# Kernel optimization log

Hardware: AMD Instinct MI355X
Metric: run time of the kernel (lower is better)

Reference implementation:

```python
import jax, jax.numpy as jnp
import numpy as np

N_NODES = 20000
N_EDGES = 320000
N_GRAPHS = 256
HIDDEN = 128
L = 4
NUM_ATOM = 28
NUM_BOND = 4
AVG_LOG = float(np.log(17.0))  # avg degree 16 -> avg_d['log']
EPS = 1e-5


def setup_inputs() -> dict:
    key = jax.random.key(0)
    ks = jax.random.split(key, 16)
    D = HIDDEN
    return {
        "x": jax.random.randint(ks[0], (N_NODES,), 0, NUM_ATOM, dtype=jnp.int32),
        "batch": jnp.sort(jax.random.randint(ks[1], (N_NODES,), 0, N_GRAPHS, dtype=jnp.int32)),
        "edge_index": jax.random.randint(ks[2], (2, N_EDGES), 0, N_NODES, dtype=jnp.int32),
        "snorm_n": jax.random.uniform(ks[3], (N_NODES, 1), dtype=jnp.float32),
        "edge_attr": jax.random.randint(ks[4], (N_EDGES,), 0, NUM_BOND, dtype=jnp.int32),
        "atom_emb": jax.random.normal(ks[5], (NUM_ATOM, D), jnp.float32) * 0.1,
        "bond_emb": jax.random.normal(ks[6], (NUM_BOND, D), jnp.float32) * 0.1,
        "pre_W": jax.random.normal(ks[7], (L, 3 * D, D), jnp.float32) / np.sqrt(3 * D),
        "pre_b": jnp.zeros((L, D), jnp.float32),
        "post_W": jax.random.normal(ks[8], (L, 13 * D, D), jnp.float32) / np.sqrt(13 * D),
        "post_b": jnp.zeros((L, D), jnp.float32),
        "mix_W": jax.random.normal(ks[9], (L, D, D), jnp.float32) / np.sqrt(D),
        "mix_b": jnp.zeros((L, D), jnp.float32),
        "bn_gamma": jnp.ones((L, D), jnp.float32),
        "bn_beta": jnp.zeros((L, D), jnp.float32),
        "r_W1": jax.random.normal(ks[10], (D, D // 2), jnp.float32) / np.sqrt(D),
        "r_b1": jnp.zeros((D // 2,), jnp.float32),
        "r_W2": jax.random.normal(ks[11], (D // 2, D // 4), jnp.float32) / np.sqrt(D // 2),
        "r_b2": jnp.zeros((D // 4,), jnp.float32),
        "r_W3": jax.random.normal(ks[12], (D // 4, 1), jnp.float32) / np.sqrt(D // 4),
        "r_b3": jnp.zeros((1,), jnp.float32),
    }


def _pna_forward(x, batch, edge_index, snorm_n, edge_attr,
                 atom_emb, bond_emb, pre_W, pre_b, post_W, post_b,
                 mix_W, mix_b, bn_gamma, bn_beta,
                 r_W1, r_b1, r_W2, r_b2, r_W3, r_b3):
    src, dst = edge_index[0], edge_index[1]
    h = atom_emb[x]                          # [N, D]
    e = bond_emb[edge_attr]                  # [E, D]
    # in-degree and PNA degree scalers (computed once)
    d = jax.ops.segment_sum(jnp.ones((src.shape[0],), h.dtype), dst, N_NODES)
    has_nb = (d > 0)[:, None]
    d_safe = jnp.maximum(d, 1.0)[:, None]
    logd = jnp.log1p(d)[:, None]
    amp = logd / AVG_LOG                     # amplification scaler
    att = AVG_LOG / jnp.maximum(logd, EPS)   # attenuation scaler
    for l in range(L):
        h_in = h
        # pretrans on edges: FC(cat(h_dst, h_src, e)) with LeakyReLU
        m = jnp.concatenate([h[dst], h[src], e], axis=-1)            # [E, 3D]
        m = jax.nn.leaky_relu(m @ pre_W[l] + pre_b[l])               # [E, D]
        # aggregators: mean, max, min, std
        mean = jax.ops.segment_sum(m, dst, N_NODES) / d_safe
        mean_sq = jax.ops.segment_sum(m * m, dst, N_NODES) / d_safe
        std = jnp.where(has_nb, jnp.sqrt(jax.nn.relu(mean_sq - mean * mean) + EPS), 0.0)
        mx = jnp.where(has_nb, jax.ops.segment_max(m, dst, N_NODES), 0.0)
        mn = jnp.where(has_nb, jax.ops.segment_min(m, dst, N_NODES), 0.0)
        agg = jnp.concatenate([mean, mx, mn, std], axis=-1)          # [N, 4D]
        agg = jnp.concatenate([agg, agg * amp, agg * att], axis=-1)  # [N, 12D]
        # posttrans FC on cat(h, agg) + mixing FC
        ph = jax.nn.leaky_relu(jnp.concatenate([h, agg], axis=-1) @ post_W[l] + post_b[l])
        ph = jax.nn.leaky_relu(ph @ mix_W[l] + mix_b[l])
        ph = ph * snorm_n                    # graph_norm
        mu = ph.mean(axis=0)                 # BatchNorm (training-mode stats)
        var = ph.var(axis=0)
        ph = bn_gamma[l] * (ph - mu) * jax.lax.rsqrt(var + EPS) + bn_beta[l]
        h = h_in + ph                        # residual
    # global mean pool per graph
    cnt = jax.ops.segment_sum(jnp.ones((x.shape[0],), h.dtype), batch, N_GRAPHS)
    g = jax.ops.segment_sum(h, batch, N_GRAPHS) / jnp.maximum(cnt, 1.0)[:, None]
    # MLPReadout: D -> D/2 -> D/4 -> 1 with ReLU
    g = jax.nn.relu(g @ r_W1 + r_b1)
    g = jax.nn.relu(g @ r_W2 + r_b2)
    return g @ r_W3 + r_b3                   # [B, 1]


def reference(x, batch, edge_index, snorm_n, edge_attr,
              atom_emb, bond_emb, pre_W, pre_b, post_W, post_b,
              mix_W, mix_b, bn_gamma, bn_beta,
              r_W1, r_b1, r_W2, r_b2, r_W3, r_b3):
    return _pna_forward(x, batch, edge_index, snorm_n, edge_attr,
                        atom_emb, bond_emb, pre_W, pre_b, post_W, post_b,
                        mix_W, mix_b, bn_gamma, bn_beta,
                        r_W1, r_b1, r_W2, r_b2, r_W3, r_b3)
```

## Files before the change

kernel.cpp:

```cpp
#include <hip/hip_runtime.h>
#include <math.h>

#define N_NODES 20000
#define N_EDGES 320000
#define N_GRAPHS 256
#define HID 128
#define NLAYERS 4
#define AVG_LOG 2.833213344056216f
#define EPS 1e-5f
#define MB64 313
#define NPAD 20032
#define SCANB 20
#define PITCH 40

typedef __attribute__((ext_vector_type(8))) short short8;
typedef __attribute__((ext_vector_type(4))) float f32x4;

static __device__ __forceinline__ float leaky(float v){ return v > 0.f ? v : 0.01f*v; }

static __device__ __forceinline__ void bsplit(float f, unsigned short& hi, unsigned short& lo){
  unsigned int u = __float_as_uint(f);
  unsigned int r = u + 0x7FFFu + ((u>>16)&1u);
  hi = (unsigned short)(r>>16);
  float hf = __uint_as_float(((unsigned int)hi)<<16);
  float l = f - hf;
  unsigned int v = __float_as_uint(l);
  unsigned int s = v + 0x7FFFu + ((v>>16)&1u);
  lo = (unsigned short)(s>>16);
}

static __device__ __forceinline__ void bsplit4(float4 f, ushort4& h, ushort4& l){
  bsplit(f.x, h.x, l.x); bsplit(f.y, h.y, l.y);
  bsplit(f.z, h.z, l.z); bsplit(f.w, h.w, l.w);
}

static __device__ __forceinline__ void gload16(const void* g, void* l){
  __builtin_amdgcn_global_load_lds((const __attribute__((address_space(1))) void*)g,
                                   (__attribute__((address_space(3))) void*)l, 16, 0, 0);
}

__global__ void k_count(const int* __restrict__ dst, int* __restrict__ deg){
  int e = blockIdx.x*blockDim.x + threadIdx.x;
  if (e < N_EDGES) atomicAdd(&deg[dst[e]], 1);
}

__global__ __launch_bounds__(1024) void k_scan1(const int* __restrict__ deg,
                                                int* __restrict__ excl, int* __restrict__ btot){
  __shared__ int buf[1024];
  int b = blockIdx.x, tid = threadIdx.x;
  int i = b*1024 + tid;
  int v = (i < N_NODES) ? deg[i] : 0;
  buf[tid] = v;
  __syncthreads();
  for (int ofs = 1; ofs < 1024; ofs <<= 1){
    int t = (tid >= ofs) ? buf[tid-ofs] : 0;
    __syncthreads();
    buf[tid] += t;
    __syncthreads();
  }
  excl[i] = buf[tid] - v;
  if (tid == 1023) btot[b] = buf[1023];
}

__global__ __launch_bounds__(1024) void k_scan2(
    const int* __restrict__ deg, const int* __restrict__ excl, const int* __restrict__ btot,
    int* __restrict__ off, float* __restrict__ invd,
    float* __restrict__ amp, float* __restrict__ att){
  __shared__ int carry_s;
  int b = blockIdx.x, tid = threadIdx.x;
  if (tid == 0){
    int c = 0;
    for (int j = 0; j < b; ++j) c += btot[j];
    carry_s = c;
  }
  __syncthreads();
  int i = b*1024 + tid;
  if (i <= N_NODES){
    off[i] = carry_s + excl[i];
    if (i < N_NODES){
      float d = (float)deg[i];
      invd[i] = 1.f / fmaxf(d, 1.f);
      float ld = log1pf(d);
      amp[i] = ld / AVG_LOG;
      att[i] = AVG_LOG / fmaxf(ld, EPS);
    }
  }
}

__global__ void k_fill(const int* __restrict__ src, const int* __restrict__ dst,
                       const int* __restrict__ eattr, const int* __restrict__ off,
                       int* __restrict__ cursor,
                       int* __restrict__ srcS, int* __restrict__ eaS){
  int e = blockIdx.x*blockDim.x + threadIdx.x;
  if (e < N_EDGES){
    int d = dst[e];
    int pos = off[d] + atomicAdd(&cursor[d], 1);
    srcS[pos] = src[e]; eaS[pos] = eattr[e];
  }
}

__global__ void k_goff(const int* __restrict__ batch, int* __restrict__ goff){
  int g = threadIdx.x;
  if (g <= N_GRAPHS){
    int lo = 0, hi = N_NODES;
    while (lo < hi){ int mid = (lo+hi)>>1; if (batch[mid] < g) lo = mid+1; else hi = mid; }
    goff[g] = lo;
  }
}

__global__ void k_hinit(const int* __restrict__ x, const float* __restrict__ atom_emb,
                        float* __restrict__ h,
                        unsigned short* __restrict__ h16h, unsigned short* __restrict__ h16l){
  int idx = blockIdx.x*blockDim.x + threadIdx.x;
  if (idx < N_NODES*32){
    int n = idx >> 5, q = idx & 31;
    float4 v = ((const float4*)atom_emb)[(size_t)x[n]*32 + q];
    ((float4*)h)[(size_t)n*32 + q] = v;
    ushort4 hh, ll; bsplit4(v, hh, ll);
    *(ushort4*)(h16h + (size_t)n*128 + q*4) = hh;
    *(ushort4*)(h16l + (size_t)n*128 + q*4) = ll;
  }
}

__global__ void k_bondall(const float* __restrict__ bond_emb, const float* __restrict__ pre_W,
                          const float* __restrict__ pre_b, float* __restrict__ BW3all){
  int l = blockIdx.x, tid = threadIdx.x;
  int r = tid >> 7, c = tid & 127;
  const float* W3 = pre_W + (size_t)l*384*128 + 256*128;
  float s = pre_b[l*128 + c];
  for (int k = 0; k < 128; ++k) s = fmaf(bond_emb[r*128 + k], W3[k*128 + c], s);
  BW3all[l*512 + tid] = s;
}

__global__ void k_wt(const float* __restrict__ pre_W, const float* __restrict__ post_W,
                     const float* __restrict__ mix_W,
                     unsigned short* __restrict__ whi, unsigned short* __restrict__ wlo){
  int y = blockIdx.y; int l = y/7, j = y%7;
  int K = (j>=3 && j<6) ? 512 : 128;
  const float* src; size_t off;
  if (j < 2)      { src = pre_W  + (size_t)l*384*128  + (size_t)j*128*128;            off = (size_t)j*16384; }
  else if (j == 2){ src = post_W + (size_t)l*1664*128;                                off = 2*16384; }
  else if (j < 6) { src = post_W + (size_t)l*1664*128 + (size_t)(128+(j-3)*512)*128;  off = 49152 + (size_t)(j-3)*65536; }
  else            { src = mix_W  + (size_t)l*128*128;                                 off = 245760; }
  unsigned short* dh = whi + (size_t)l*262144 + off;
  unsigned short* dl = wlo + (size_t)l*262144 + off;
  int kq8 = K/8;
  int ntask = 128*kq8;
  int t = blockIdx.x*256 + threadIdx.x;
  if (t >= ntask) return;
  int c  = t / kq8;
  int k0 = (t % kq8)*8;
  unsigned short h8[8] __attribute__((aligned(16)));
  unsigned short l8[8] __attribute__((aligned(16)));
  #pragma unroll
  for (int i=0;i<8;++i) bsplit(src[(size_t)(k0+i)*128 + c], h8[i], l8[i]);
  *(uint4*)(dh + (size_t)c*K + k0) = *(const uint4*)h8;
  *(uint4*)(dl + (size_t)c*K + k0) = *(const uint4*)l8;
}

template<int MODE>
__global__ __launch_bounds__(256) void k_mf16(
    const unsigned short* __restrict__ whi, const unsigned short* __restrict__ wlo,
    const unsigned short* __restrict__ Ahg, const unsigned short* __restrict__ Alg,
    float* __restrict__ out)
{
  const int K    = (MODE==1) ? 512 : 128;
  const int ASTR = (MODE==1) ? 512 : 128;
  const int OSTR = (MODE==1) ? 384 : 128;
  __shared__ unsigned short Ah[64*32], Al[64*32], Bh[128*32], Bl[128*32];
  int tid = threadIdx.x;
  int lane = tid & 63;
  int wv = tid >> 6;
  int wm = (wv>>1)*32, wn = (wv&1)*64;
  int y = blockIdx.x % 3;
  int mbase = (blockIdx.x / 3) * 64;
  const unsigned short* wh = whi + (size_t)y*K*128;
  const unsigned short* wl = wlo + (size_t)y*K*128;
  float* outp = out; int ocol = 0;
  if (MODE == 0) outp = out + (size_t)y*(size_t)N_NODES*128;
  if (MODE == 1) ocol = y*128;

  int lq = lane >> 2, ls = lane & 3;
  int kg = ls ^ (lq & 3) ^ ((lq >> 2) & 3);
  int a_row = wv*16 + lq;
  const unsigned short* agh = Ahg + (size_t)(mbase + a_row)*ASTR + kg*8;
  const unsigned short* agl = Alg + (size_t)(mbase + a_row)*ASTR + kg*8;
  unsigned short* a_ldsh = Ah + wv*512;
  unsigned short* a_ldsl = Al + wv*512;
  int b_col0 = (wv*2+0)*16 + lq;
  int b_col1 = (wv*2+1)*16 + lq;
  const unsigned short* bgh0 = wh + (size_t)b_col0*K + kg*8;
  const unsigned short* bgh1 = wh + (size_t)b_col1*K + kg*8;
  const unsigned short* bgl0 = wl + (size_t)b_col0*K + kg*8;
  const unsigned short* bgl1 = wl + (size_t)b_col1*K + kg*8;
  unsigned short* b_ldsh0 = Bh + (wv*2+0)*512;
  unsigned short* b_ldsh1 = Bh + (wv*2+1)*512;
  unsigned short* b_ldsl0 = Bl + (wv*2+0)*512;
  unsigned short* b_ldsl1 = Bl + (wv*2+1)*512;

  f32x4 acc[2][4];
  #pragma unroll
  for (int mi=0;mi<2;++mi)
    #pragma unroll
    for (int ni=0;ni<4;++ni)
      acc[mi][ni] = (f32x4){0.f,0.f,0.f,0.f};

  int lr = lane & 15, lk = lane >> 4;
  int sl = lk ^ (lr & 3) ^ ((lr >> 2) & 3);

  for (int kt = 0; kt < K; kt += 32){
    gload16(agh + kt, a_ldsh);
    gload16(agl + kt, a_ldsl);
    gload16(bgh0 + kt, b_ldsh0);
    gload16(bgh1 + kt, b_ldsh1);
    gload16(bgl0 + kt, b_ldsl0);
    gload16(bgl1 + kt, b_ldsl1);
    __syncthreads();
    short8 ah[2], al2[2], bh4[4], bl4[4];
    #pragma unroll
    for (int mi=0;mi<2;++mi){
      int idx = (wm + mi*16 + lr)*32 + sl*8;
      ah[mi]  = *(const short8*)(Ah + idx);
      al2[mi] = *(const short8*)(Al + idx);
    }
    #pragma unroll
    for (int ni=0;ni<4;++ni){
      int idx = (wn + ni*16 + lr)*32 + sl*8;
      bh4[ni] = *(const short8*)(Bh + idx);
      bl4[ni] = *(const short8*)(Bl + idx);
    }
    #pragma unroll
    for (int mi=0;mi<2;++mi){
      #pragma unroll
      for (int ni=0;ni<4;++ni){
        acc[mi][ni] = __builtin_amdgcn_mfma_f32_16x16x32_bf16(ah[mi],  bh4[ni], acc[mi][ni], 0,0,0);
        acc[mi][ni] = __builtin_amdgcn_mfma_f32_16x16x32_bf16(ah[mi],  bl4[ni], acc[mi][ni], 0,0,0);
        acc[mi][ni] = __builtin_amdgcn_mfma_f32_16x16x32_bf16(al2[mi], bh4[ni], acc[mi][ni], 0,0,0);
      }
    }
    __syncthreads();
  }

  #pragma unroll
  for (int mi=0;mi<2;++mi){
    #pragma unroll
    for (int ni=0;ni<4;++ni){
      int gcol = wn + ni*16 + lr;
      #pragma unroll
      for (int r=0;r<4;++r){
        int grow = mbase + wm + mi*16 + lk*4 + r;
        if (grow < N_NODES)
          outp[(size_t)grow*OSTR + ocol + gcol] = acc[mi][ni][r];
      }
    }
  }
}

__global__ __launch_bounds__(256) void k_mix(
    const unsigned short* __restrict__ wh, const unsigned short* __restrict__ wl,
    const float* __restrict__ Yh, const float* __restrict__ Yamt,
    const float* __restrict__ amp, const float* __restrict__ att,
    const float* __restrict__ post_b, const float* __restrict__ mix_b,
    const float* __restrict__ snorm,
    float* __restrict__ tb, float* __restrict__ bnpart)
{
  __shared__ unsigned short Ah[64*PITCH], Al[64*PITCH], Bh[128*PITCH], Bl[128*PITCH];
  __shared__ float bns[2][128], bnq[2][128];
  int tid = threadIdx.x;
  int lane = tid & 63;
  int wv = tid >> 6;
  int wm = (wv>>1)*32, wn = (wv&1)*64;
  int mbase = blockIdx.x*64;

  int a_row = tid >> 2, a_kg = tid & 3;
  int a_nrow = min(mbase + a_row, N_NODES-1);
  float av = amp[a_nrow], tv2 = att[a_nrow];
  const float* yhp = Yh   + (size_t)a_nrow*128;
  const float* yap = Yamt + (size_t)a_nrow*384;
  unsigned short* a_dh = Ah + a_row*PITCH + a_kg*8;
  unsigned short* a_dl = Al + a_row*PITCH + a_kg*8;

  f32x4 acc[2][4];
  #pragma unroll
  for (int mi=0;mi<2;++mi)
    #pragma unroll
    for (int ni=0;ni<4;++ni)
      acc[mi][ni] = (f32x4){0.f,0.f,0.f,0.f};

  int lr = lane & 15, lk = lane >> 4;

  for (int kt = 0; kt < 128; kt += 32){
    #pragma unroll
    for (int i=0;i<2;++i){
      int s = tid + 256*i;
      int col = s >> 2, kgg = s & 3;
      *(uint4*)(Bh + col*PITCH + kgg*8) = *(const uint4*)(wh + (size_t)col*128 + kt + kgg*8);
      *(uint4*)(Bl + col*PITCH + kgg*8) = *(const uint4*)(wl + (size_t)col*128 + kt + kgg*8);
    }
    {
      int c0 = kt + a_kg*8;
      float4 h0 = *(const float4*)(yhp + c0),       h1 = *(const float4*)(yhp + c0 + 4);
      float4 a0 = *(const float4*)(yap + c0),       a1 = *(const float4*)(yap + c0 + 4);
      float4 m0 = *(const float4*)(yap + 128 + c0), m1 = *(const float4*)(yap + 132 + c0);
      float4 t0 = *(const float4*)(yap + 256 + c0), t1 = *(const float4*)(yap + 260 + c0);
      float4 p0 = *(const float4*)(post_b + c0),    p1 = *(const float4*)(post_b + c0 + 4);
      float fv[8];
      fv[0] = leaky(h0.x + a0.x + av*m0.x + tv2*t0.x + p0.x);
      fv[1] = leaky(h0.y + a0.y + av*m0.y + tv2*t0.y + p0.y);
      fv[2] = leaky(h0.z + a0.z + av*m0.z + tv2*t0.z + p0.z);
      fv[3] = leaky(h0.w + a0.w + av*m0.w + tv2*t0.w + p0.w);
      fv[4] = leaky(h1.x + a1.x + av*m1.x + tv2*t1.x + p1.x);
      fv[5] = leaky(h1.y + a1.y + av*m1.y + tv2*t1.y + p1.y);
      fv[6] = leaky(h1.z + a1.z + av*m1.z + tv2*t1.z + p1.z);
      fv[7] = leaky(h1.w + a1.w + av*m1.w + tv2*t1.w + p1.w);
      unsigned short h8[8] __attribute__((aligned(16)));
      unsigned short l8[8] __attribute__((aligned(16)));
      #pragma unroll
      for (int i=0;i<8;++i) bsplit(fv[i], h8[i], l8[i]);
      *(uint4*)a_dh = *(const uint4*)h8;
      *(uint4*)a_dl = *(const uint4*)l8;
    }
    __syncthreads();
    short8 ah[2], al2[2], bh4[4], bl4[4];
    #pragma unroll
    for (int mi=0;mi<2;++mi){
      int idx = (wm + mi*16 + lr)*PITCH + lk*8;
      ah[mi]  = *(const short8*)(Ah + idx);
      al2[mi] = *(const short8*)(Al + idx);
    }
    #pragma unroll
    for (int ni=0;ni<4;++ni){
      int idx = (wn + ni*16 + lr)*PITCH + lk*8;
      bh4[ni] = *(const short8*)(Bh + idx);
      bl4[ni] = *(const short8*)(Bl + idx);
    }
    #pragma unroll
    for (int mi=0;mi<2;++mi){
      #pragma unroll
      for (int ni=0;ni<4;++ni){
        acc[mi][ni] = __builtin_amdgcn_mfma_f32_16x16x32_bf16(ah[mi],  bh4[ni], acc[mi][ni], 0,0,0);
        acc[mi][ni] = __builtin_amdgcn_mfma_f32_16x16x32_bf16(ah[mi],  bl4[ni], acc[mi][ni], 0,0,0);
        acc[mi][ni] = __builtin_amdgcn_mfma_f32_16x16x32_bf16(al2[mi], bh4[ni], acc[mi][ni], 0,0,0);
      }
    }
    __syncthreads();
  }

  float sn[2][4]; bool vld[2][4];
  #pragma unroll
  for (int mi=0;mi<2;++mi)
    #pragma unroll
    for (int r=0;r<4;++r){
      int grow = mbase + wm + mi*16 + lk*4 + r;
      vld[mi][r] = (grow < N_NODES);
      sn[mi][r] = vld[mi][r] ? snorm[grow] : 0.f;
    }
  int half = wv >> 1;
  #pragma unroll
  for (int ni=0;ni<4;++ni){
    int gcol = wn + ni*16 + lr;
    float bv = mix_b[gcol];
    float s = 0.f, q = 0.f;
    #pragma unroll
    for (int mi=0;mi<2;++mi){
      #pragma unroll
      for (int r=0;r<4;++r){
        if (vld[mi][r]){
          int grow = mbase + wm + mi*16 + lk*4 + r;
          float v = leaky(acc[mi][ni][r] + bv) * sn[mi][r];
          tb[(size_t)grow*128 + gcol] = v;
          s += v; q += v*v;
        }
      }
    }
    s += __shfl_xor(s, 16); s += __shfl_xor(s, 32);
    q += __shfl_xor(q, 16); q += __shfl_xor(q, 32);
    if (lk == 0){ bns[half][gcol] = s; bnq[half][gcol] = q; }
  }
  __syncthreads();
  if (tid < 128){
    bnpart[(size_t)blockIdx.x*256 + tid]       = bns[0][tid] + bns[1][tid];
    bnpart[(size_t)blockIdx.x*256 + 128 + tid] = bnq[0][tid] + bnq[1][tid];
  }
}

__global__ __launch_bounds__(256) void k_fusedagg(
    const float* __restrict__ H1, const float* __restrict__ H2,
    const float* __restrict__ BW3,
    const int* __restrict__ srcS, const int* __restrict__ eaS,
    const int* __restrict__ off, const float* __restrict__ invd,
    unsigned short* __restrict__ aggh, unsigned short* __restrict__ aggl)
{
  __shared__ float bw[4][128];
  int tid = threadIdx.x;
  bw[tid>>7][tid&127]     = BW3[tid];
  bw[2+(tid>>7)][tid&127] = BW3[256+tid];
  __syncthreads();

  int node = blockIdx.x*8 + (tid>>5);
  int q = tid & 31;
  float4 c4 = ((const float4*)(H1 + (size_t)node*HID))[q];
  int s = off[node], e = off[node+1];
  float4 sum = make_float4(0,0,0,0), sq = make_float4(0,0,0,0);
  float4 mx = make_float4(-3.4e38f,-3.4e38f,-3.4e38f,-3.4e38f);
  float4 mn = make_float4( 3.4e38f, 3.4e38f, 3.4e38f, 3.4e38f);

  #define FA_BODY(T,B) { \
    float vx = leaky(c4.x + T.x + B.x); \
    float vy = leaky(c4.y + T.y + B.y); \
    float vz = leaky(c4.z + T.z + B.z); \
    float vw = leaky(c4.w + T.w + B.w); \
    sum.x += vx; sum.y += vy; sum.z += vz; sum.w += vw; \
    sq.x += vx*vx; sq.y += vy*vy; sq.z += vz*vz; sq.w += vw*vw; \
    mx.x = fmaxf(mx.x, vx); mx.y = fmaxf(mx.y, vy); mx.z = fmaxf(mx.z, vz); mx.w = fmaxf(mx.w, vw); \
    mn.x = fminf(mn.x, vx); mn.y = fminf(mn.y, vy); mn.z = fminf(mn.z, vz); mn.w = fminf(mn.w, vw); }

  int i = s;
  for (; i + 1 < e; i += 2){
    int sv0 = srcS[i],   ev0 = eaS[i];
    int sv1 = srcS[i+1], ev1 = eaS[i+1];
    float4 t0 = ((const float4*)(H2 + (size_t)sv0*HID))[q];
    float4 t1 = ((const float4*)(H2 + (size_t)sv1*HID))[q];
    float4 b0 = ((const float4*)(&bw[ev0][0]))[q];
    float4 b1 = ((const float4*)(&bw[ev1][0]))[q];
    FA_BODY(t0,b0)
    FA_BODY(t1,b1)
  }
  if (i < e){
    int sv = srcS[i], ev = eaS[i];
    float4 t  = ((const float4*)(H2 + (size_t)sv*HID))[q];
    float4 b4 = ((const float4*)(&bw[ev][0]))[q];
    FA_BODY(t,b4)
  }
  #undef FA_BODY

  bool has = (e > s);
  float iv = invd[node];
  float4 mean = make_float4(sum.x*iv, sum.y*iv, sum.z*iv, sum.w*iv);
  float4 msq  = make_float4(sq.x*iv,  sq.y*iv,  sq.z*iv,  sq.w*iv);
  float4 sd;
  sd.x = has ? sqrtf(fmaxf(msq.x - mean.x*mean.x, 0.f) + EPS) : 0.f;
  sd.y = has ? sqrtf(fmaxf(msq.y - mean.y*mean.y, 0.f) + EPS) : 0.f;
  sd.z = has ? sqrtf(fmaxf(msq.z - mean.z*mean.z, 0.f) + EPS) : 0.f;
  sd.w = has ? sqrtf(fmaxf(msq.w - mean.w*mean.w, 0.f) + EPS) : 0.f;
  if (!has){ mx = make_float4(0,0,0,0); mn = make_float4(0,0,0,0); }
  size_t base = (size_t)node*512 + q*4;
  ushort4 hh, ll;
  bsplit4(mean, hh, ll);
  *(ushort4*)(aggh + base      ) = hh; *(ushort4*)(aggl + base      ) = ll;
  bsplit4(mx, hh, ll);
  *(ushort4*)(aggh + base + 128) = hh; *(ushort4*)(aggl + base + 128) = ll;
  bsplit4(mn, hh, ll);
  *(ushort4*)(aggh + base + 256) = hh; *(ushort4*)(aggl + base + 256) = ll;
  bsplit4(sd, hh, ll);
  *(ushort4*)(aggh + base + 384) = hh; *(ushort4*)(aggl + base + 384) = ll;
}

__global__ __launch_bounds__(512) void k_bnfinal(const float* __restrict__ bnpart,
                                                 float* __restrict__ mu, float* __restrict__ rstd){
  __shared__ double ss[4][128], qq[4][128];
  int tid = threadIdx.x;
  int c = tid & 127, p = tid >> 7;
  double s = 0.0, q = 0.0;
  for (int b = p; b < MB64; b += 4){
    s += (double)bnpart[(size_t)b*256 + c];
    q += (double)bnpart[(size_t)b*256 + 128 + c];
  }
  ss[p][c] = s; qq[p][c] = q;
  __syncthreads();
  if (p == 0){
    double S = ss[0][c] + ss[1][c] + ss[2][c] + ss[3][c];
    double Q = qq[0][c] + qq[1][c] + qq[2][c] + qq[3][c];
    double mean = S / (double)N_NODES;
    double var  = Q / (double)N_NODES - mean*mean;
    mu[c] = (float)mean;
    rstd[c] = rsqrtf((float)var + EPS);
  }
}

__global__ void k_apply(const float* __restrict__ t, const float* __restrict__ mu,
                        const float* __restrict__ rstd, const float* __restrict__ gamma,
                        const float* __restrict__ beta, float* __restrict__ h,
                        unsigned short* __restrict__ h16h, unsigned short* __restrict__ h16l){
  int idx = blockIdx.x*blockDim.x + threadIdx.x;
  if (idx < N_NODES*32){
    int n = idx >> 5, q = idx & 31;
    float4 tv = ((const float4*)t)[(size_t)n*32 + q];
    float4 hv = ((float4*)h)[(size_t)n*32 + q];
    float4 g4 = ((const float4*)gamma)[q], b4 = ((const float4*)beta)[q];
    float4 m4 = ((const float4*)mu)[q],    r4 = ((const float4*)rstd)[q];
    hv.x += g4.x*(tv.x-m4.x)*r4.x + b4.x;
    hv.y += g4.y*(tv.y-m4.y)*r4.y + b4.y;
    hv.z += g4.z*(tv.z-m4.z)*r4.z + b4.z;
    hv.w += g4.w*(tv.w-m4.w)*r4.w + b4.w;
    ((float4*)h)[(size_t)n*32 + q] = hv;
    ushort4 hh, ll; bsplit4(hv, hh, ll);
    *(ushort4*)(h16h + (size_t)n*128 + q*4) = hh;
    *(ushort4*)(h16l + (size_t)n*128 + q*4) = ll;
  }
}

__global__ __launch_bounds__(128) void k_poolread(
    const int* __restrict__ goff, const float* __restrict__ h,
    const float* __restrict__ W1, const float* __restrict__ b1,
    const float* __restrict__ W2, const float* __restrict__ b2,
    const float* __restrict__ W3, const float* __restrict__ b3,
    float* __restrict__ out){
  __shared__ float gl[128];
  __shared__ float a1[64];
  __shared__ float a2[32];
  int g = blockIdx.x, tid = threadIdx.x;
  int s = goff[g], e = goff[g+1];
  float sum = 0.f;
  for (int r = s; r < e; ++r) sum += h[(size_t)r*128 + tid];
  gl[tid] = sum / fmaxf((float)(e - s), 1.f);
  __syncthreads();
  if (tid < 64){
    float s1 = b1[tid];
    for (int k = 0; k < 128; ++k) s1 = fmaf(gl[k], W1[k*64 + tid], s1);
    a1[tid] = fmaxf(s1, 0.f);
  }
  __syncthreads();
  if (tid < 32){
    float s2 = b2[tid];
    for (int k = 0; k < 64; ++k) s2 = fmaf(a1[k], W2[k*32 + tid], s2);
    a2[tid] = fmaxf(s2, 0.f);
  }
  __syncthreads();
  if (tid == 0){
    float s3 = b3[0];
    for (int k = 0; k < 32; ++k) s3 = fmaf(a2[k], W3[k], s3);
    out[g] = s3;
  }
}

extern "C" void kernel_launch(void* const* d_in, const int* in_sizes, int n_in,
                              void* d_out, int out_size, void* d_ws, size_t ws_size,
                              hipStream_t stream) {
  const int*   x        = (const int*)  d_in[0];
  const int*   batch    = (const int*)  d_in[1];
  const int*   ei       = (const int*)  d_in[2];
  const float* snorm    = (const float*)d_in[3];
  const int*   eattr    = (const int*)  d_in[4];
  const float* atom_emb = (const float*)d_in[5];
  const float* bond_emb = (const float*)d_in[6];
  const float* pre_W    = (const float*)d_in[7];
  const float* pre_b    = (const float*)d_in[8];
  const float* post_W   = (const float*)d_in[9];
  const float* post_b   = (const float*)d_in[10];
  const float* mix_W    = (const float*)d_in[11];
  const float* mix_b    = (const float*)d_in[12];
  const float* bn_g     = (const float*)d_in[13];
  const float* bn_b     = (const float*)d_in[14];
  const float* rW1      = (const float*)d_in[15];
  const float* rb1      = (const float*)d_in[16];
  const float* rW2      = (const float*)d_in[17];
  const float* rb2      = (const float*)d_in[18];
  const float* rW3      = (const float*)d_in[19];
  const float* rb3      = (const float*)d_in[20];
  float* outp = (float*)d_out;

  const int* srcI = ei;
  const int* dstI = ei + N_EDGES;

  char* ws = (char*)d_ws;
  size_t o = 0;
  auto alloc = [&](size_t bytes)->char* {
    char* p = ws + o;
    o = (o + bytes + 255) & ~(size_t)255;
    return p;
  };
  int*    deg    = (int*)   alloc((size_t)N_NODES*4);
  int*    cursor = (int*)   alloc((size_t)N_NODES*4);
  int*    excl   = (int*)   alloc((size_t)SCANB*1024*4);
  int*    btot   = (int*)   alloc((size_t)SCANB*4);
  int*    off    = (int*)   alloc((size_t)(N_NODES+1)*4);
  int*    goff   = (int*)   alloc((size_t)(N_GRAPHS+1)*4);
  int*    srcS   = (int*)   alloc((size_t)N_EDGES*4);
  int*    eaS    = (int*)   alloc((size_t)N_EDGES*4);
  float*  invd   = (float*) alloc((size_t)N_NODES*4);
  float*  ampb   = (float*) alloc((size_t)N_NODES*4);
  float*  attb   = (float*) alloc((size_t)N_NODES*4);
  float*  h      = (float*) alloc((size_t)N_NODES*HID*4);
  float*  H3     = (float*) alloc((size_t)3*N_NODES*HID*4);
  float*  Yamt   = (float*) alloc((size_t)N_NODES*384*4);
  float*  BW3all = (float*) alloc((size_t)NLAYERS*512*4);
  float*  tb     = (float*) alloc((size_t)N_NODES*HID*4);
  unsigned short* whi  = (unsigned short*)alloc((size_t)NLAYERS*262144*2);
  unsigned short* wlo  = (unsigned short*)alloc((size_t)NLAYERS*262144*2);
  unsigned short* h16h = (unsigned short*)alloc((size_t)NPAD*128*2);
  unsigned short* h16l = (unsigned short*)alloc((size_t)NPAD*128*2);
  unsigned short* aggh = (unsigned short*)alloc((size_t)NPAD*512*2);
  unsigned short* aggl = (unsigned short*)alloc((size_t)NPAD*512*2);
  float*  bnpart = (float*) alloc((size_t)MB64*256*4);
  float*  mu     = (float*) alloc(128*4);
  float*  rstd   = (float*) alloc(128*4);

  hipMemsetAsync(deg, 0, (size_t)((char*)cursor - (char*)deg) + (size_t)N_NODES*4, stream);
  k_count<<<(N_EDGES+255)/256, 256, 0, stream>>>(dstI, deg);
  k_scan1<<<SCANB, 1024, 0, stream>>>(deg, excl, btot);
  k_scan2<<<SCANB, 1024, 0, stream>>>(deg, excl, btot, off, invd, ampb, attb);
  k_fill<<<(N_EDGES+255)/256, 256, 0, stream>>>(srcI, dstI, eattr, off, cursor, srcS, eaS);
  k_goff<<<1, 512, 0, stream>>>(batch, goff);
  k_hinit<<<(N_NODES*32+255)/256, 256, 0, stream>>>(x, atom_emb, h, h16h, h16l);
  k_wt<<<dim3(32, NLAYERS*7), 256, 0, stream>>>(pre_W, post_W, mix_W, whi, wlo);
  k_bondall<<<NLAYERS, 512, 0, stream>>>(bond_emb, pre_W, pre_b, BW3all);

  float* H1 = H3;
  float* H2 = H3 + (size_t)N_NODES*HID;
  float* Yh = H3 + (size_t)2*N_NODES*HID;
  for (int l = 0; l < NLAYERS; ++l){
    const unsigned short* whl = whi + (size_t)l*262144;
    const unsigned short* wll = wlo + (size_t)l*262144;
    k_mf16<0><<<MB64*3, 256, 0, stream>>>(whl, wll, h16h, h16l, H3);
    k_fusedagg<<<N_NODES/8, 256, 0, stream>>>(H1, H2, BW3all + (size_t)l*512,
        srcS, eaS, off, invd, aggh, aggl);
    k_mf16<1><<<MB64*3, 256, 0, stream>>>(whl + 49152, wll + 49152, aggh, aggl, Yamt);
    k_mix<<<MB64, 256, 0, stream>>>(whl + 245760, wll + 245760,
        Yh, Yamt, ampb, attb, post_b + (size_t)l*128, mix_b + (size_t)l*128,
        snorm, tb, bnpart);
    k_bnfinal<<<1, 512, 0, stream>>>(bnpart, mu, rstd);
    k_apply<<<(N_NODES*32+255)/256, 256, 0, stream>>>(tb, mu, rstd,
        bn_g + (size_t)l*128, bn_b + (size_t)l*128, h, h16h, h16l);
  }

  k_poolread<<<N_GRAPHS, 128, 0, stream>>>(goff, h, rW1, rb1, rW2, rb2, rW3, rb3, outp);
}
```

Measured before the change: 611.9 us.

## Fuse BatchNorm finalize and residual apply into next GEMM prologue and pooling

Drops the per-layer BN finalize and apply kernels. BN statistics are now accumulated with double-precision atomics directly from k_mix. The next layer's pre-GEMM computes mean and rstd, applies BN plus the residual to h, and bf16-splits the A tile in its prologue. Ping-pong h buffers let one block column write the updated h, and the last layer's BN apply moves into the pooling kernel. This removes launches and the separate full passes over h and the bf16 copies of h. In exchange, each of the three column blocks rereads and re-splits the same A rows, and the atomics add contention.

```diff
diff --git a/kernel.cpp b/kernel.cpp
--- a/kernel.cpp
+++ b/kernel.cpp
@@ -11,7 +11,6 @@
 #define MB64 313
 #define NPAD 20032
 #define SCANB 20
-#define PITCH 40
 
 typedef __attribute__((ext_vector_type(8))) short short8;
 typedef __attribute__((ext_vector_type(4))) float f32x4;
@@ -109,16 +108,11 @@
 }
 
 __global__ void k_hinit(const int* __restrict__ x, const float* __restrict__ atom_emb,
-                        float* __restrict__ h,
-                        unsigned short* __restrict__ h16h, unsigned short* __restrict__ h16l){
+                        float* __restrict__ h){
   int idx = blockIdx.x*blockDim.x + threadIdx.x;
   if (idx < N_NODES*32){
     int n = idx >> 5, q = idx & 31;
-    float4 v = ((const float4*)atom_emb)[(size_t)x[n]*32 + q];
-    ((float4*)h)[(size_t)n*32 + q] = v;
-    ushort4 hh, ll; bsplit4(v, hh, ll);
-    *(ushort4*)(h16h + (size_t)n*128 + q*4) = hh;
-    *(ushort4*)(h16l + (size_t)n*128 + q*4) = ll;
+    ((float4*)h)[(size_t)n*32 + q] = ((const float4*)atom_emb)[(size_t)x[n]*32 + q];
   }
 }
 
@@ -158,15 +152,154 @@
   *(uint4*)(dl + (size_t)c*K + k0) = *(const uint4*)l8;
 }
 
-template<int MODE>
-__global__ __launch_bounds__(256) void k_mf16(
+template<int FIRST>
+__global__ __launch_bounds__(256) void k_mf0(
+    const unsigned short* __restrict__ whi, const unsigned short* __restrict__ wlo,
+    const float* __restrict__ hin, float* __restrict__ hout,
+    const float* __restrict__ tb, const double* __restrict__ bnsum,
+    const float* __restrict__ gamma, const float* __restrict__ beta,
+    float* __restrict__ out)
+{
+  const int K = 128;
+  __shared__ unsigned short Ah[4*64*32], Al[4*64*32];
+  __shared__ unsigned short Bh[128*32], Bl[128*32];
+  __shared__ float muS[128], rsS[128], gS[128], bS[128];
+  int tid = threadIdx.x, lane = tid & 63, wv = tid >> 6;
+  int wm = (wv>>1)*32, wn = (wv&1)*64;
+  int y = blockIdx.x % 3;
+  int mbase = (blockIdx.x / 3) * 64;
+  const unsigned short* wh = whi + (size_t)y*K*128;
+  const unsigned short* wl = wlo + (size_t)y*K*128;
+  float* outp = out + (size_t)y*(size_t)N_NODES*128;
+
+  if (!FIRST){
+    if (tid < 128){
+      double mean = bnsum[tid] / (double)N_NODES;
+      double var  = bnsum[128+tid] / (double)N_NODES - mean*mean;
+      muS[tid] = (float)mean;
+      rsS[tid] = rsqrtf((float)var + EPS);
+      gS[tid]  = gamma[tid];
+      bS[tid]  = beta[tid];
+    }
+    __syncthreads();
+  }
+
+  {
+    int arow = tid >> 2, kq = tid & 3;
+    int ag = mbase + arow;
+    int acl = min(ag, N_NODES-1);
+    float hv[32];
+    const float* hp = hin + (size_t)acl*128 + kq*32;
+    #pragma unroll
+    for (int i=0;i<8;++i) *(float4*)&hv[i*4] = *(const float4*)(hp + i*4);
+    if (!FIRST){
+      const float* tp = tb + (size_t)acl*128 + kq*32;
+      #pragma unroll
+      for (int i=0;i<8;++i){
+        float4 t4 = *(const float4*)(tp + i*4);
+        int c = kq*32 + i*4;
+        hv[i*4+0] += gS[c+0]*(t4.x - muS[c+0])*rsS[c+0] + bS[c+0];
+        hv[i*4+1] += gS[c+1]*(t4.y - muS[c+1])*rsS[c+1] + bS[c+1];
+        hv[i*4+2] += gS[c+2]*(t4.z - muS[c+2])*rsS[c+2] + bS[c+2];
+        hv[i*4+3] += gS[c+3]*(t4.w - muS[c+3])*rsS[c+3] + bS[c+3];
+      }
+      if (y == 0 && ag < N_NODES){
+        float* hw = hout + (size_t)ag*128 + kq*32;
+        #pragma unroll
+        for (int i=0;i<8;++i) *(float4*)(hw + i*4) = *(const float4*)&hv[i*4];
+      }
+    }
+    int f = (arow & 3) ^ ((arow >> 2) & 3);
+    unsigned short* aH = Ah + kq*2048 + arow*32;
+    unsigned short* aL = Al + kq*2048 + arow*32;
+    #pragma unroll
+    for (int j=0;j<4;++j){
+      int slot = j ^ f;
+      unsigned short hh8[8] __attribute__((aligned(16)));
+      unsigned short ll8[8] __attribute__((aligned(16)));
+      #pragma unroll
+      for (int e=0;e<8;++e) bsplit(hv[j*8+e], hh8[e], ll8[e]);
+      *(uint4*)(aH + slot*8) = *(const uint4*)hh8;
+      *(uint4*)(aL + slot*8) = *(const uint4*)ll8;
+    }
+  }
+
+  int lq = lane >> 2, ls = lane & 3;
+  int kg = ls ^ (lq & 3) ^ ((lq >> 2) & 3);
+  int b_col0 = (wv*2+0)*16 + lq;
+  int b_col1 = (wv*2+1)*16 + lq;
+  const unsigned short* bgh0 = wh + (size_t)b_col0*K + kg*8;
+  const unsigned short* bgh1 = wh + (size_t)b_col1*K + kg*8;
+  const unsigned short* bgl0 = wl + (size_t)b_col0*K + kg*8;
+  const unsigned short* bgl1 = wl + (size_t)b_col1*K + kg*8;
+  unsigned short* b_ldsh0 = Bh + (wv*2+0)*512;
+  unsigned short* b_ldsh1 = Bh + (wv*2+1)*512;
+  unsigned short* b_ldsl0 = Bl + (wv*2+0)*512;
+  unsigned short* b_ldsl1 = Bl + (wv*2+1)*512;
+
+  f32x4 acc[2][4];
+  #pragma unroll
+  for (int mi=0;mi<2;++mi)
+    #pragma unroll
+    for (int ni=0;ni<4;++ni)
+      acc[mi][ni] = (f32x4){0.f,0.f,0.f,0.f};
+
+  int lr = lane & 15, lk = lane >> 4;
+  int sl = lk ^ (lr & 3) ^ ((lr >> 2) & 3);
+
+  for (int kt = 0; kt < K; kt += 32){
+    gload16(bgh0 + kt, b_ldsh0);
+    gload16(bgh1 + kt, b_ldsh1);
+    gload16(bgl0 + kt, b_ldsl0);
+    gload16(bgl1 + kt, b_ldsl1);
+    __syncthreads();
+    int win = kt >> 5;
+    short8 ah[2], al2[2], bh4[4], bl4[4];
+    #pragma unroll
+    for (int mi=0;mi<2;++mi){
+      int idx = win*2048 + (wm + mi*16 + lr)*32 + sl*8;
+      ah[mi]  = *(const short8*)(Ah + idx);
+      al2[mi] = *(const short8*)(Al + idx);
+    }
+    #pragma unroll
+    for (int ni=0;ni<4;++ni){
+      int idx = (wn + ni*16 + lr)*32 + sl*8;
+      bh4[ni] = *(const short8*)(Bh + idx);
+      bl4[ni] = *(const short8*)(Bl + idx);
+    }
+    #pragma unroll
+    for (int mi=0;mi<2;++mi){
+      #pragma unroll
+      for (int ni=0;ni<4;++ni){
+        acc[mi][ni] = __builtin_amdgcn_mfma_f32_16x16x32_bf16(ah[mi],  bh4[ni], acc[mi][ni], 0,0,0);
+        acc[mi][ni] = __builtin_amdgcn_mfma_f32_16x16x32_bf16(ah[mi],  bl4[ni], acc[mi][ni], 0,0,0);
+        acc[mi][ni] = __builtin_amdgcn_mfma_f32_16x16x32_bf16(al2[mi], bh4[ni], acc[mi][ni], 0,0,0);
+      }
+    }
+    __syncthreads();
+  }
+
+  #pragma unroll
+  for (int mi=0;mi<2;++mi){
+    #pragma unroll
+    for (int ni=0;ni<4;++ni){
+      int gcol = wn + ni*16 + lr;
+      #pragma unroll
+      for (int r=0;r<4;++r){
+        int grow = mbase + wm + mi*16 + lk*4 + r;
+        if (grow < N_NODES)
+          outp[(size_t)grow*128 + gcol] = acc[mi][ni][r];
+      }
+    }
+  }
+}
+
+__global__ __launch_bounds__(256) void k_mf1(
     const unsigned short* __restrict__ whi, const unsigned short* __restrict__ wlo,
     const unsigned short* __restrict__ Ahg, const unsigned short* __restrict__ Alg,
     float* __restrict__ out)
 {
-  const int K    = (MODE==1) ? 512 : 128;
-  const int ASTR = (MODE==1) ? 512 : 128;
-  const int OSTR = (MODE==1) ? 384 : 128;
+  const int K = 512;
   __shared__ unsigned short Ah[64*32], Al[64*32], Bh[128*32], Bl[128*32];
   int tid = threadIdx.x;
   int lane = tid & 63;
@@ -176,15 +309,13 @@
   int mbase = (blockIdx.x / 3) * 64;
   const unsigned short* wh = whi + (size_t)y*K*128;
   const unsigned short* wl = wlo + (size_t)y*K*128;
-  float* outp = out; int ocol = 0;
-  if (MODE == 0) outp = out + (size_t)y*(size_t)N_NODES*128;
-  if (MODE == 1) ocol = y*128;
+  int ocol = y*128;
 
   int lq = lane >> 2, ls = lane & 3;
   int kg = ls ^ (lq & 3) ^ ((lq >> 2) & 3);
   int a_row = wv*16 + lq;
-  const unsigned short* agh = Ahg + (size_t)(mbase + a_row)*ASTR + kg*8;
-  const unsigned short* agl = Alg + (size_t)(mbase + a_row)*ASTR + kg*8;
+  const unsigned short* agh = Ahg + (size_t)(mbase + a_row)*512 + kg*8;
+  const unsigned short* agl = Alg + (size_t)(mbase + a_row)*512 + kg*8;
   unsigned short* a_ldsh = Ah + wv*512;
   unsigned short* a_ldsl = Al + wv*512;
   int b_col0 = (wv*2+0)*16 + lq;
@@ -250,19 +381,20 @@
       for (int r=0;r<4;++r){
         int grow = mbase + wm + mi*16 + lk*4 + r;
         if (grow < N_NODES)
-          outp[(size_t)grow*OSTR + ocol + gcol] = acc[mi][ni][r];
+          out[(size_t)grow*384 + ocol + gcol] = acc[mi][ni][r];
       }
     }
   }
 }
 
+#define PITCH 40
 __global__ __launch_bounds__(256) void k_mix(
     const unsigned short* __restrict__ wh, const unsigned short* __restrict__ wl,
     const float* __restrict__ Yh, const float* __restrict__ Yamt,
     const float* __restrict__ amp, const float* __restrict__ att,
     const float* __restrict__ post_b, const float* __restrict__ mix_b,
     const float* __restrict__ snorm,
-    float* __restrict__ tb, float* __restrict__ bnpart)
+    float* __restrict__ tb, double* __restrict__ bnsum)
 {
   __shared__ unsigned short Ah[64*PITCH], Al[64*PITCH], Bh[128*PITCH], Bl[128*PITCH];
   __shared__ float bns[2][128], bnq[2][128];
@@ -379,8 +511,8 @@
   }
   __syncthreads();
   if (tid < 128){
-    bnpart[(size_t)blockIdx.x*256 + tid]       = bns[0][tid] + bns[1][tid];
-    bnpart[(size_t)blockIdx.x*256 + 128 + tid] = bnq[0][tid] + bnq[1][tid];
+    atomicAdd(&bnsum[tid],       (double)(bns[0][tid] + bns[1][tid]));
+    atomicAdd(&bnsum[128 + tid], (double)(bnq[0][tid] + bnq[1][tid]));
   }
 }
 
@@ -456,52 +588,10 @@
   *(ushort4*)(aggh + base + 384) = hh; *(ushort4*)(aggl + base + 384) = ll;
 }
 
-__global__ __launch_bounds__(512) void k_bnfinal(const float* __restrict__ bnpart,
-                                                 float* __restrict__ mu, float* __restrict__ rstd){
-  __shared__ double ss[4][128], qq[4][128];
-  int tid = threadIdx.x;
-  int c = tid & 127, p = tid >> 7;
-  double s = 0.0, q = 0.0;
-  for (int b = p; b < MB64; b += 4){
-    s += (double)bnpart[(size_t)b*256 + c];
-    q += (double)bnpart[(size_t)b*256 + 128 + c];
-  }
-  ss[p][c] = s; qq[p][c] = q;
-  __syncthreads();
-  if (p == 0){
-    double S = ss[0][c] + ss[1][c] + ss[2][c] + ss[3][c];
-    double Q = qq[0][c] + qq[1][c] + qq[2][c] + qq[3][c];
-    double mean = S / (double)N_NODES;
-    double var  = Q / (double)N_NODES - mean*mean;
-    mu[c] = (float)mean;
-    rstd[c] = rsqrtf((float)var + EPS);
-  }
-}
-
-__global__ void k_apply(const float* __restrict__ t, const float* __restrict__ mu,
-                        const float* __restrict__ rstd, const float* __restrict__ gamma,
-                        const float* __restrict__ beta, float* __restrict__ h,
-                        unsigned short* __restrict__ h16h, unsigned short* __restrict__ h16l){
-  int idx = blockIdx.x*blockDim.x + threadIdx.x;
-  if (idx < N_NODES*32){
-    int n = idx >> 5, q = idx & 31;
-    float4 tv = ((const float4*)t)[(size_t)n*32 + q];
-    float4 hv = ((float4*)h)[(size_t)n*32 + q];
-    float4 g4 = ((const float4*)gamma)[q], b4 = ((const float4*)beta)[q];
-    float4 m4 = ((const float4*)mu)[q],    r4 = ((const float4*)rstd)[q];
-    hv.x += g4.x*(tv.x-m4.x)*r4.x + b4.x;
-    hv.y += g4.y*(tv.y-m4.y)*r4.y + b4.y;
-    hv.z += g4.z*(tv.z-m4.z)*r4.z + b4.z;
-    hv.w += g4.w*(tv.w-m4.w)*r4.w + b4.w;
-    ((float4*)h)[(size_t)n*32 + q] = hv;
-    ushort4 hh, ll; bsplit4(hv, hh, ll);
-    *(ushort4*)(h16h + (size_t)n*128 + q*4) = hh;
-    *(ushort4*)(h16l + (size_t)n*128 + q*4) = ll;
-  }
-}
-
 __global__ __launch_bounds__(128) void k_poolread(
     const int* __restrict__ goff, const float* __restrict__ h,
+    const float* __restrict__ tb, const double* __restrict__ bnsum,
+    const float* __restrict__ gamma, const float* __restrict__ beta,
     const float* __restrict__ W1, const float* __restrict__ b1,
     const float* __restrict__ W2, const float* __restrict__ b2,
     const float* __restrict__ W3, const float* __restrict__ b3,
@@ -510,9 +600,17 @@
   __shared__ float a1[64];
   __shared__ float a2[32];
   int g = blockIdx.x, tid = threadIdx.x;
+  double mean = bnsum[tid] / (double)N_NODES;
+  double var  = bnsum[128+tid] / (double)N_NODES - mean*mean;
+  float mu = (float)mean;
+  float rs = rsqrtf((float)var + EPS);
+  float gm = gamma[tid], bt = beta[tid];
   int s = goff[g], e = goff[g+1];
   float sum = 0.f;
-  for (int r = s; r < e; ++r) sum += h[(size_t)r*128 + tid];
+  for (int r = s; r < e; ++r){
+    float v = h[(size_t)r*128 + tid] + gm*(tb[(size_t)r*128 + tid] - mu)*rs + bt;
+    sum += v;
+  }
   gl[tid] = sum / fmaxf((float)(e - s), 1.f);
   __syncthreads();
   if (tid < 64){
@@ -570,39 +668,37 @@
     o = (o + bytes + 255) & ~(size_t)255;
     return p;
   };
-  int*    deg    = (int*)   alloc((size_t)N_NODES*4);
-  int*    cursor = (int*)   alloc((size_t)N_NODES*4);
-  int*    excl   = (int*)   alloc((size_t)SCANB*1024*4);
-  int*    btot   = (int*)   alloc((size_t)SCANB*4);
-  int*    off    = (int*)   alloc((size_t)(N_NODES+1)*4);
-  int*    goff   = (int*)   alloc((size_t)(N_GRAPHS+1)*4);
-  int*    srcS   = (int*)   alloc((size_t)N_EDGES*4);
-  int*    eaS    = (int*)   alloc((size_t)N_EDGES*4);
-  float*  invd   = (float*) alloc((size_t)N_NODES*4);
-  float*  ampb   = (float*) alloc((size_t)N_NODES*4);
-  float*  attb   = (float*) alloc((size_t)N_NODES*4);
-  float*  h      = (float*) alloc((size_t)N_NODES*HID*4);
-  float*  H3     = (float*) alloc((size_t)3*N_NODES*HID*4);
-  float*  Yamt   = (float*) alloc((size_t)N_NODES*384*4);
-  float*  BW3all = (float*) alloc((size_t)NLAYERS*512*4);
-  float*  tb     = (float*) alloc((size_t)N_NODES*HID*4);
+  int*    deg     = (int*)   alloc((size_t)N_NODES*4);
+  int*    cursor  = (int*)   alloc((size_t)N_NODES*4);
+  double* bnsumA  = (double*)alloc((size_t)NLAYERS*256*8);
+  int*    excl    = (int*)   alloc((size_t)SCANB*1024*4);
+  int*    btot    = (int*)   alloc((size_t)SCANB*4);
+  int*    off     = (int*)   alloc((size_t)(N_NODES+1)*4);
+  int*    goff    = (int*)   alloc((size_t)(N_GRAPHS+1)*4);
+  int*    srcS    = (int*)   alloc((size_t)N_EDGES*4);
+  int*    eaS     = (int*)   alloc((size_t)N_EDGES*4);
+  float*  invd    = (float*) alloc((size_t)N_NODES*4);
+  float*  ampb    = (float*) alloc((size_t)N_NODES*4);
+  float*  attb    = (float*) alloc((size_t)N_NODES*4);
+  float*  hP0     = (float*) alloc((size_t)N_NODES*HID*4);
+  float*  hP1     = (float*) alloc((size_t)N_NODES*HID*4);
+  float*  H3      = (float*) alloc((size_t)3*N_NODES*HID*4);
+  float*  Yamt    = (float*) alloc((size_t)N_NODES*384*4);
+  float*  BW3all  = (float*) alloc((size_t)NLAYERS*512*4);
+  float*  tb      = (float*) alloc((size_t)N_NODES*HID*4);
   unsigned short* whi  = (unsigned short*)alloc((size_t)NLAYERS*262144*2);
   unsigned short* wlo  = (unsigned short*)alloc((size_t)NLAYERS*262144*2);
-  unsigned short* h16h = (unsigned short*)alloc((size_t)NPAD*128*2);
-  unsigned short* h16l = (unsigned short*)alloc((size_t)NPAD*128*2);
   unsigned short* aggh = (unsigned short*)alloc((size_t)NPAD*512*2);
   unsigned short* aggl = (unsigned short*)alloc((size_t)NPAD*512*2);
-  float*  bnpart = (float*) alloc((size_t)MB64*256*4);
-  float*  mu     = (float*) alloc(128*4);
-  float*  rstd   = (float*) alloc(128*4);
-
-  hipMemsetAsync(deg, 0, (size_t)((char*)cursor - (char*)deg) + (size_t)N_NODES*4, stream);
+
+  hipMemsetAsync(deg, 0,
+      (size_t)((char*)bnsumA - (char*)deg) + (size_t)NLAYERS*256*8, stream);
   k_count<<<(N_EDGES+255)/256, 256, 0, stream>>>(dstI, deg);
   k_scan1<<<SCANB, 1024, 0, stream>>>(deg, excl, btot);
   k_scan2<<<SCANB, 1024, 0, stream>>>(deg, excl, btot, off, invd, ampb, attb);
   k_fill<<<(N_EDGES+255)/256, 256, 0, stream>>>(srcI, dstI, eattr, off, cursor, srcS, eaS);
   k_goff<<<1, 512, 0, stream>>>(batch, goff);
-  k_hinit<<<(N_NODES*32+255)/256, 256, 0, stream>>>(x, atom_emb, h, h16h, h16l);
+  k_hinit<<<(N_NODES*32+255)/256, 256, 0, stream>>>(x, atom_emb, hP0);
   k_wt<<<dim3(32, NLAYERS*7), 256, 0, stream>>>(pre_W, post_W, mix_W, whi, wlo);
   k_bondall<<<NLAYERS, 512, 0, stream>>>(bond_emb, pre_W, pre_b, BW3all);
 
@@ -612,17 +708,24 @@
   for (int l = 0; l < NLAYERS; ++l){
     const unsigned short* whl = whi + (size_t)l*262144;
     const unsigned short* wll = wlo + (size_t)l*262144;
-    k_mf16<0><<<MB64*3, 256, 0, stream>>>(whl, wll, h16h, h16l, H3);
+    float* hin  = (l == 0) ? hP0 : (((l & 1) == 1) ? hP0 : hP1);
+    float* hout = ((l & 1) == 1) ? hP1 : hP0;
+    if (l == 0)
+      k_mf0<1><<<MB64*3, 256, 0, stream>>>(whl, wll, hP0, nullptr,
+          nullptr, bnsumA, bn_g, bn_b, H3);
+    else
+      k_mf0<0><<<MB64*3, 256, 0, stream>>>(whl, wll, hin, hout,
+          tb, bnsumA + (size_t)(l-1)*256, bn_g + (size_t)(l-1)*128,
+          bn_b + (size_t)(l-1)*128, H3);
     k_fusedagg<<<N_NODES/8, 256, 0, stream>>>(H1, H2, BW3all + (size_t)l*512,
         srcS, eaS, off, invd, aggh, aggl);
-    k_mf16<1><<<MB64*3, 256, 0, stream>>>(whl + 49152, wll + 49152, aggh, aggl, Yamt);
+    k_mf1<<<MB64*3, 256, 0, stream>>>(whl + 49152, wll + 49152, aggh, aggl, Yamt);
     k_mix<<<MB64, 256, 0, stream>>>(whl + 245760, wll + 245760,
         Yh, Yamt, ampb, attb, post_b + (size_t)l*128, mix_b + (size_t)l*128,
-        snorm, tb, bnpart);
-    k_bnfinal<<<1, 512, 0, stream>>>(bnpart, mu, rstd);
-    k_apply<<<(N_NODES*32+255)/256, 256, 0, stream>>>(tb, mu, rstd,
-        bn_g + (size_t)l*128, bn_b + (size_t)l*128, h, h16h, h16l);
-  }
-
-  k_poolread<<<N_GRAPHS, 128, 0, stream>>>(goff, h, rW1, rb1, rW2, rb2, rW3, rb3, outp);
-}
+        snorm, tb, bnsumA + (size_t)l*256);
+  }
+
+  k_poolread<<<N_GRAPHS, 128, 0, stream>>>(goff, hP1, tb,
+      bnsumA + (size_t)3*256, bn_g + (size_t)3*128, bn_b + (size_t)3*128,
+      rW1, rb1, rW2, rb2, rW3, rb3, outp);
+}
```

Measured after the change: 555.0 us (median of 2 runs). 1.1x faster.
